# Performance work log

Measured on AMD Instinct MI355X. Metric: run time of the kernel, lower is better.

Reference implementation:

```python
import jax, jax.numpy as jnp
import numpy as np
from jax import lax

B, S, D, F = 2, 4096, 1024, 4096
LN_EPS = 1e-6

def _layer_norm(x, scale, bias):
    mu = jnp.mean(x, axis=-1, keepdims=True)
    var = jnp.mean(jnp.square(x - mu), axis=-1, keepdims=True)
    return (x - mu) * lax.rsqrt(var + LN_EPS) * scale + bias

def _gate_loop(q, k, v, a):
    # max-headed GateLoop: one head per channel, scalar complex state per channel
    # h_t = a_t * h_{t-1} + k_t * v_t ; y_t = q_t * h_t
    kv = (k * v).astype(jnp.complex64)
    def comb(e1, e2):
        a1, x1 = e1
        a2, x2 = e2
        return (a1 * a2, a2 * x1 + x2)
    _, h = lax.associative_scan(comb, (a, kv), axis=1)
    return q.astype(jnp.complex64) * h

def setup_inputs() -> dict:
    key = jax.random.key(0)
    ks = jax.random.split(key, 12)
    sd = 1.0 / np.sqrt(D)
    sf = 1.0 / np.sqrt(F)
    return {
        "x": jax.random.normal(ks[0], (B, S, D), jnp.float32),
        "Wq": jax.random.normal(ks[1], (D, D), jnp.float32) * sd,
        "Wk": jax.random.normal(ks[2], (D, D), jnp.float32) * sd,
        "Wv": jax.random.normal(ks[3], (D, D), jnp.float32) * sd,
        "Wa": jax.random.normal(ks[4], (D, 2 * D), jnp.float32) * sd,
        "Wg": jax.random.normal(ks[5], (D, D), jnp.float32) * sd,
        "Wo": jax.random.normal(ks[6], (D, D), jnp.float32) * sd,
        "ln1_scale": jnp.ones((D,), jnp.float32),
        "ln1_bias": jnp.zeros((D,), jnp.float32),
        "W1": jax.random.normal(ks[7], (D, F), jnp.float32) * sd,
        "b1": jax.random.normal(ks[8], (F,), jnp.float32) * 1e-6,
        "W2": jax.random.normal(ks[9], (F, D), jnp.float32) * sf,
        "b2": jax.random.normal(ks[10], (D,), jnp.float32) * 1e-6,
        "ln2_scale": jnp.ones((D,), jnp.float32),
        "ln2_bias": jnp.zeros((D,), jnp.float32),
    }

def reference(x, Wq, Wk, Wv, Wa, Wg, Wo, ln1_scale, ln1_bias, W1, b1, W2, b2, ln2_scale, ln2_bias):
    q = x @ Wq
    k = x @ Wk
    v = x @ Wv
    a = x @ Wa
    a_real, a_imag = jnp.split(a, 2, axis=-1)
    a_c = a_real + 1j * a_imag
    magnitude = jnp.abs(a_c)
    phase = jnp.angle(a_c)
    a_c = jax.nn.sigmoid(magnitude).astype(jnp.complex64) * jnp.exp(1j * phase)
    g = x.astype(jnp.complex64) @ Wg.astype(jnp.complex64)
    y = _gate_loop(q, k, v, a_c)
    y = y * (g * jax.nn.sigmoid(g))  # silu on complex g
    y = y @ Wo.astype(jnp.complex64)
    y = y.real
    # dropout deterministic (training=False)
    y = _layer_norm(y + x, ln1_scale, ln1_bias)
    h = jax.nn.gelu(y @ W1 + b1)
    out = h @ W2 + b2
    out = _layer_norm(out + y, ln2_scale, ln2_bias)
    return out
```

## Files before the change

### kernel.cpp

```cpp
#include <hip/hip_runtime.h>
#include <cstdint>

typedef unsigned short u16;
typedef unsigned int u32;

#define AS1 __attribute__((address_space(1)))
#define AS3 __attribute__((address_space(3)))

typedef _Float16 f16x8 __attribute__((ext_vector_type(8)));
typedef float f32x4 __attribute__((ext_vector_type(4)));

static constexpr int Bb = 2, Ss = 4096, Dd = 1024, Ff = 4096;
static constexpr int Mtok = Bb * Ss;
static constexpr int NCH = 128;
static constexpr int TCH = Ss / NCH;
static constexpr int PW = 6144;

__device__ __forceinline__ float h2f(u16 u) {
    union { u16 u; _Float16 h; } w; w.u = u; return (float)w.h;
}
__device__ __forceinline__ u16 f2h(float f) {
    union { _Float16 h; u16 u; } w; w.h = (_Float16)f; return w.u;
}

__device__ __forceinline__ void gload_lds16(const u16* g, u16* l) {
    __builtin_amdgcn_global_load_lds((const AS1 u32*)g, (AS3 u32*)l, 16, 0, 0);
}

__global__ __launch_bounds__(256) void cvt_f32_f16(const float* __restrict__ src,
                                                   u16* __restrict__ dst) {
    const long i = ((long)blockIdx.x * 256 + threadIdx.x) * 4;
    float4 f = *(const float4*)(src + i);
    ushort4 o;
    o.x = f2h(f.x); o.y = f2h(f.y); o.z = f2h(f.z); o.w = f2h(f.w);
    *(ushort4*)(dst + i) = o;
}

__global__ __launch_bounds__(1024) void transpose_f32_f16(const float* __restrict__ src,
                                                          u16* __restrict__ dst,
                                                          int K, int N) {
    __shared__ u16 t[32][33];
    const int tx = threadIdx.x, ty = threadIdx.y;
    const int n0 = blockIdx.x * 32, k0 = blockIdx.y * 32;
    t[ty][tx] = f2h(src[(long)(k0 + ty) * N + n0 + tx]);
    __syncthreads();
    dst[(long)(n0 + ty) * K + k0 + tx] = t[tx][ty];
}

template <int EPI>
__global__ __launch_bounds__(512, 2) void gemm8p(const u16* __restrict__ A,
                                                 const u16* __restrict__ BT,
                                                 u16* __restrict__ C,
                                                 const float* __restrict__ bias,
                                                 int M, int N, int K,
                                                 int lda, int ldc) {
    extern __shared__ u16 lds[];
    const int tid = threadIdx.x;

    const int ntn = N >> 8;
    int bid = blockIdx.x;
    {
        const int cpx = gridDim.x >> 3;
        bid = (bid & 7) * cpx + (bid >> 3);
    }
    const int tm = (bid / ntn) << 8;
    const int tn = (bid % ntn) << 8;

    const int srow = tid >> 3;
    const int scol = ((tid & 7) ^ (srow & 7)) << 3;
    const u16* Abase = A + (long)(tm + srow) * lda + scol;
    const u16* Bbase = BT + (long)(tn + srow) * (long)K + scol;
    const long lda64 = (long)lda << 6;
    const long ldb64 = (long)K << 6;

    const int nt = K >> 6;

    auto stA = [&](u16* bufbase, int h, int kt) {
        u16* d = bufbase + h * 8192 + tid * 8;
        const u16* g = Abase + (long)(h * 128) * lda + (kt << 6);
        gload_lds16(g, d);
        gload_lds16(g + lda64, d + 4096);
    };
    auto stB = [&](u16* bufbase, int h, int kt) {
        u16* d = bufbase + 16384 + h * 8192 + tid * 8;
        const u16* g = Bbase + (long)(h * 128) * (long)K + (kt << 6);
        gload_lds16(g, d);
        gload_lds16(g + ldb64, d + 4096);
    };

    const int wid = tid >> 6, lane = tid & 63;
    const int r16 = lane & 15, q = lane >> 4;
    const int wm = (wid >> 2) * 128;
    const int wn = (wid & 3) * 64;
    const int r7 = r16 & 7;
    const int cx0 = (q ^ r7) << 3;
    const int cx1 = ((4 | q) ^ r7) << 3;
    const int aoff = (wm + r16) * 64;
    const int boff = 16384 + (wn + r16) * 64;

    f32x4 acc[8][4];
#pragma unroll
    for (int i = 0; i < 8; i++)
#pragma unroll
        for (int j = 0; j < 4; j++) acc[i][j] = (f32x4){0.f, 0.f, 0.f, 0.f};

    {
        const int t1 = nt > 1 ? 1 : 0;
        stA(lds, 0, 0);
        stA(lds, 1, 0);
        stB(lds, 0, 0);
        stB(lds, 1, 0);
        stB(lds + 32768, 0, t1);
        stB(lds + 32768, 1, t1);
    }

    for (int it = 0; it < nt; ++it) {
        u16* sb = lds + ((it & 1) << 15);
        u16* so = lds + (((it & 1) ^ 1) << 15);
        const int tA = (it + 1 < nt) ? it + 1 : nt - 1;
        const int tB = (it + 2 < nt) ? it + 2 : nt - 1;

        asm volatile("s_waitcnt vmcnt(4)" ::: "memory");
        __builtin_amdgcn_s_barrier();

        f16x8 vb[4][2];
#pragma unroll
        for (int ni = 0; ni < 4; ni++) {
            vb[ni][0] = *(const f16x8*)(sb + boff + ni * 1024 + cx0);
            vb[ni][1] = *(const f16x8*)(sb + boff + ni * 1024 + cx1);
        }

#pragma unroll
        for (int p = 0; p < 4; ++p) {
            f16x8 pa[2][2];
#pragma unroll
            for (int m2 = 0; m2 < 2; m2++) {
                pa[m2][0] = *(const f16x8*)(sb + aoff + (2 * p + m2) * 1024 + cx0);
                pa[m2][1] = *(const f16x8*)(sb + aoff + (2 * p + m2) * 1024 + cx1);
            }
            if (p == 0)      stA(so, 0, tA);
            else if (p == 1) stA(so, 1, tA);
            else if (p == 2) stB(sb, 0, tB);
            else             stB(sb, 1, tB);
            __builtin_amdgcn_s_barrier();
            asm volatile("s_waitcnt lgkmcnt(0)" ::: "memory");
            __builtin_amdgcn_s_setprio(1);
#pragma unroll
            for (int m2 = 0; m2 < 2; m2++)
#pragma unroll
                for (int ni = 0; ni < 4; ni++) {
                    acc[2 * p + m2][ni] = __builtin_amdgcn_mfma_f32_16x16x32_f16(
                        pa[m2][0], vb[ni][0], acc[2 * p + m2][ni], 0, 0, 0);
                    acc[2 * p + m2][ni] = __builtin_amdgcn_mfma_f32_16x16x32_f16(
                        pa[m2][1], vb[ni][1], acc[2 * p + m2][ni], 0, 0, 0);
                }
            __builtin_amdgcn_s_setprio(0);
            __builtin_amdgcn_s_barrier();
        }
    }

    asm volatile("s_waitcnt vmcnt(0)" ::: "memory");

#pragma unroll
    for (int mi = 0; mi < 8; mi++) {
#pragma unroll
        for (int ni = 0; ni < 4; ni++) {
            const int gcol = tn + wn + ni * 16 + r16;
            float bv = 0.f;
            if (EPI) bv = bias[gcol];
#pragma unroll
            for (int j = 0; j < 4; j++) {
                const int grow = tm + wm + mi * 16 + q * 4 + j;
                float v = acc[mi][ni][j];
                if (EPI) v += bv;
                if (EPI == 1) {
                    float t = tanhf(0.7978845608028654f * (v + 0.044715f * v * v * v));
                    v = 0.5f * v * (1.0f + t);
                }
                C[(long)grow * ldc + gcol] = f2h(v);
            }
        }
    }
}

template <int EPI>
__global__ __launch_bounds__(512, 2) void gemm8p_n128(const u16* __restrict__ A,
                                                      const u16* __restrict__ BT,
                                                      u16* __restrict__ C,
                                                      const float* __restrict__ bias,
                                                      int M, int N, int K,
                                                      int lda, int ldc) {
    extern __shared__ u16 lds[];
    const int tid = threadIdx.x;

    const int ntn = N >> 7;
    int bid = blockIdx.x;
    {
        const int cpx = gridDim.x >> 3;
        bid = (bid & 7) * cpx + (bid >> 3);
    }
    const int tm = (bid / ntn) << 8;
    const int tn = (bid % ntn) << 7;

    const int srow = tid >> 3;
    const int scol = ((tid & 7) ^ (srow & 7)) << 3;
    const u16* Abase = A + (long)(tm + srow) * lda + scol;
    const u16* Bbase = BT + (long)(tn + srow) * (long)K + scol;
    const long lda64 = (long)lda << 6;
    const long ldb64 = (long)K << 6;

    const int nt = K >> 6;

    auto stA = [&](u16* bufbase, int h, int kt) {
        u16* d = bufbase + h * 8192 + tid * 8;
        const u16* g = Abase + (long)(h * 128) * lda + (kt << 6);
        gload_lds16(g, d);
        gload_lds16(g + lda64, d + 4096);
    };
    auto stB = [&](u16* bufbase, int kt) {
        u16* d = bufbase + 16384 + tid * 8;
        const u16* g = Bbase + (kt << 6);
        gload_lds16(g, d);
        gload_lds16(g + ldb64, d + 4096);
    };

    const int wid = tid >> 6, lane = tid & 63;
    const int r16 = lane & 15, q = lane >> 4;
    const int wm = (wid >> 1) * 64;
    const int wn = (wid & 1) * 64;
    const int r7 = r16 & 7;
    const int cx0 = (q ^ r7) << 3;
    const int cx1 = ((4 | q) ^ r7) << 3;
    const int aoff = (wm + r16) * 64;
    const int boff = 16384 + (wn + r16) * 64;

    f32x4 acc[4][4];
#pragma unroll
    for (int i = 0; i < 4; i++)
#pragma unroll
        for (int j = 0; j < 4; j++) acc[i][j] = (f32x4){0.f, 0.f, 0.f, 0.f};

    {
        const int t1 = nt > 1 ? 1 : 0;
        stA(lds, 0, 0);
        stA(lds, 1, 0);
        stB(lds, 0);
        stB(lds + 24576, t1);
    }

    for (int it = 0; it < nt; ++it) {
        u16* sb = lds + (it & 1) * 24576;
        u16* so = lds + ((it & 1) ^ 1) * 24576;
        const int tA = (it + 1 < nt) ? it + 1 : nt - 1;
        const int tB = (it + 2 < nt) ? it + 2 : nt - 1;

        asm volatile("s_waitcnt vmcnt(2)" ::: "memory");
        __builtin_amdgcn_s_barrier();

        f16x8 vb[4][2];
#pragma unroll
        for (int ni = 0; ni < 4; ni++) {
            vb[ni][0] = *(const f16x8*)(sb + boff + ni * 1024 + cx0);
            vb[ni][1] = *(const f16x8*)(sb + boff + ni * 1024 + cx1);
        }

#pragma unroll
        for (int p = 0; p < 2; ++p) {
            f16x8 pa[2][2];
#pragma unroll
            for (int m2 = 0; m2 < 2; m2++) {
                pa[m2][0] = *(const f16x8*)(sb + aoff + (2 * p + m2) * 1024 + cx0);
                pa[m2][1] = *(const f16x8*)(sb + aoff + (2 * p + m2) * 1024 + cx1);
            }
            if (p == 0) {
                stA(so, 0, tA);
            } else {
                stA(so, 1, tA);
                stB(sb, tB);
            }
            __builtin_amdgcn_s_barrier();
            asm volatile("s_waitcnt lgkmcnt(0)" ::: "memory");
            __builtin_amdgcn_s_setprio(1);
#pragma unroll
            for (int m2 = 0; m2 < 2; m2++)
#pragma unroll
                for (int ni = 0; ni < 4; ni++) {
                    acc[2 * p + m2][ni] = __builtin_amdgcn_mfma_f32_16x16x32_f16(
                        pa[m2][0], vb[ni][0], acc[2 * p + m2][ni], 0, 0, 0);
                    acc[2 * p + m2][ni] = __builtin_amdgcn_mfma_f32_16x16x32_f16(
                        pa[m2][1], vb[ni][1], acc[2 * p + m2][ni], 0, 0, 0);
                }
            __builtin_amdgcn_s_setprio(0);
            __builtin_amdgcn_s_barrier();
        }
    }

    asm volatile("s_waitcnt vmcnt(0)" ::: "memory");

#pragma unroll
    for (int mi = 0; mi < 4; mi++) {
#pragma unroll
        for (int ni = 0; ni < 4; ni++) {
            const int gcol = tn + wn + ni * 16 + r16;
            float bv = 0.f;
            if (EPI) bv = bias[gcol];
#pragma unroll
            for (int j = 0; j < 4; j++) {
                const int grow = tm + wm + mi * 16 + q * 4 + j;
                float v = acc[mi][ni][j];
                if (EPI) v += bv;
                if (EPI == 1) {
                    float t = tanhf(0.7978845608028654f * (v + 0.044715f * v * v * v));
                    v = 0.5f * v * (1.0f + t);
                }
                C[(long)grow * ldc + gcol] = f2h(v);
            }
        }
    }
}

__device__ __forceinline__ void a_transform(float ar, float ai, float& cr, float& ci) {
    float m = sqrtf(ar * ar + ai * ai);
    float sg = 1.f / (1.f + __expf(-m));
    float sc = sg / fmaxf(m, 1e-30f);
    cr = ar * sc;
    ci = ai * sc;
}

__global__ __launch_bounds__(1024) void scan1(const u16* __restrict__ pcat,
                                              float4* __restrict__ sum4) {
    const int b = blockIdx.y, c = blockIdx.x, d = threadIdx.x;
    float Arp = 1.f, Aip = 0.f, Xr = 0.f, Xi = 0.f;
    const long rowbase = (long)b * Ss + (long)c * TCH;
#pragma unroll 4
    for (int s = 0; s < TCH; ++s) {
        const long ro = (rowbase + s) * PW;
        float ar = h2f(pcat[ro + 3072 + d]);
        float ai = h2f(pcat[ro + 4096 + d]);
        float kk = h2f(pcat[ro + 1024 + d]);
        float vv = h2f(pcat[ro + 2048 + d]);
        float cr, ci;
        a_transform(ar, ai, cr, ci);
        float kv = kk * vv;
        float nXr = cr * Xr - ci * Xi + kv;
        float nXi = cr * Xi + ci * Xr;
        Xr = nXr; Xi = nXi;
        float nAr = cr * Arp - ci * Aip;
        float nAi = cr * Aip + ci * Arp;
        Arp = nAr; Aip = nAi;
    }
    sum4[((long)b * NCH + c) * 1024 + d] = make_float4(Arp, Aip, Xr, Xi);
}

__global__ __launch_bounds__(256) void scan2(const float4* __restrict__ sum4,
                                             float2* __restrict__ carry) {
    const int idx = blockIdx.x * 256 + threadIdx.x;
    const int b = idx >> 10, d = idx & 1023;
    float hr = 0.f, hi = 0.f;
    for (int cb = 0; cb < NCH / 8; ++cb) {
        float4 t[8];
#pragma unroll
        for (int j = 0; j < 8; j++)
            t[j] = sum4[((long)b * NCH + cb * 8 + j) * 1024 + d];
#pragma unroll
        for (int j = 0; j < 8; j++) {
            carry[((long)b * NCH + cb * 8 + j) * 1024 + d] = make_float2(hr, hi);
            float nr = t[j].x * hr - t[j].y * hi + t[j].z;
            float ni = t[j].x * hi + t[j].y * hr + t[j].w;
            hr = nr; hi = ni;
        }
    }
}

__global__ __launch_bounds__(1024) void scan3(u16* pcat,
                                              const float2* __restrict__ carry) {
    const int b = blockIdx.y, c = blockIdx.x, d = threadIdx.x;
    float2 h0 = carry[((long)b * NCH + c) * 1024 + d];
    float hr = h0.x, hi = h0.y;
    const long rowbase = (long)b * Ss + (long)c * TCH;
#pragma unroll 4
    for (int s = 0; s < TCH; ++s) {
        const long ro = (rowbase + s) * PW;
        float ar = h2f(pcat[ro + 3072 + d]);
        float ai = h2f(pcat[ro + 4096 + d]);
        float kk = h2f(pcat[ro + 1024 + d]);
        float vv = h2f(pcat[ro + 2048 + d]);
        float cr, ci;
        a_transform(ar, ai, cr, ci);
        float kv = kk * vv;
        float nhr = cr * hr - ci * hi + kv;
        float nhi = cr * hi + ci * hr;
        hr = nhr; hi = nhi;
        float gg = h2f(pcat[ro + 5120 + d]);
        float si = gg / (1.f + __expf(-gg));
        float yv = h2f(pcat[ro + d]) * hr * si;
        pcat[ro + d] = f2h(yv);
    }
}

template <int RESF32, int OUTF32>
__global__ __launch_bounds__(256) void ln_kernel(const u16* __restrict__ a, int sa,
                                                 const void* __restrict__ bres, int sres,
                                                 const float* __restrict__ scale,
                                                 const float* __restrict__ bias,
                                                 void* __restrict__ out, int sout) {
    const int row = blockIdx.x;
    const int tid = threadIdx.x;
    const long abase = (long)row * sa;
    const long rbase = (long)row * sres;
    const long obase = (long)row * sout;
    float v[4];
#pragma unroll
    for (int j = 0; j < 4; j++) {
        int d = tid * 4 + j;
        float rb = RESF32 ? ((const float*)bres)[rbase + d]
                          : h2f(((const u16*)bres)[rbase + d]);
        v[j] = h2f(a[abase + d]) + rb;
    }
    float s = v[0] + v[1] + v[2] + v[3];
    float s2 = v[0] * v[0] + v[1] * v[1] + v[2] * v[2] + v[3] * v[3];
#pragma unroll
    for (int off = 32; off; off >>= 1) {
        s += __shfl_down(s, off);
        s2 += __shfl_down(s2, off);
    }
    __shared__ float red[8];
    const int w = tid >> 6, lane = tid & 63;
    if (lane == 0) { red[w] = s; red[4 + w] = s2; }
    __syncthreads();
    if (tid == 0) {
        float ts = red[0] + red[1] + red[2] + red[3];
        float ts2 = red[4] + red[5] + red[6] + red[7];
        float mu = ts * (1.f / 1024.f);
        float var = ts2 * (1.f / 1024.f) - mu * mu;
        red[0] = mu;
        red[1] = rsqrtf(var + 1e-6f);
    }
    __syncthreads();
    const float mu = red[0], rs = red[1];
#pragma unroll
    for (int j = 0; j < 4; j++) {
        int d = tid * 4 + j;
        float y = (v[j] - mu) * rs * scale[d] + bias[d];
        if (OUTF32) ((float*)out)[obase + d] = y;
        else        ((u16*)out)[obase + d] = f2h(y);
    }
}

extern "C" void kernel_launch(void* const* d_in, const int* in_sizes, int n_in,
                              void* d_out, int out_size, void* d_ws, size_t ws_size,
                              hipStream_t stream) {
    const float* x    = (const float*)d_in[0];
    const float* Wq   = (const float*)d_in[1];
    const float* Wk   = (const float*)d_in[2];
    const float* Wv   = (const float*)d_in[3];
    const float* Wa   = (const float*)d_in[4];
    const float* Wg   = (const float*)d_in[5];
    const float* Wo   = (const float*)d_in[6];
    const float* ln1s = (const float*)d_in[7];
    const float* ln1b = (const float*)d_in[8];
    const float* W1   = (const float*)d_in[9];
    const float* b1   = (const float*)d_in[10];
    const float* W2   = (const float*)d_in[11];
    const float* b2   = (const float*)d_in[12];
    const float* ln2s = (const float*)d_in[13];
    const float* ln2b = (const float*)d_in[14];

    u16* ws    = (u16*)d_ws;
    u16* xb    = ws;
    u16* WTcat = xb + (8u << 20);
    u16* WTo   = WTcat + (6u << 20);
    u16* WT1   = WTo + (1u << 20);
    u16* WT2   = WT1 + (4u << 20);
    u16* pcat  = WT2 + (4u << 20);

    float4* sum4  = (float4*)WTcat;
    float2* carry = (float2*)(WTcat + (2u << 20));

    static bool attr_done = false;
    if (!attr_done) {
        hipFuncSetAttribute(reinterpret_cast<const void*>(&gemm8p<0>),
                            hipFuncAttributeMaxDynamicSharedMemorySize, 131072);
        hipFuncSetAttribute(reinterpret_cast<const void*>(&gemm8p<1>),
                            hipFuncAttributeMaxDynamicSharedMemorySize, 131072);
        hipFuncSetAttribute(reinterpret_cast<const void*>(&gemm8p_n128<0>),
                            hipFuncAttributeMaxDynamicSharedMemorySize, 98304);
        hipFuncSetAttribute(reinterpret_cast<const void*>(&gemm8p_n128<2>),
                            hipFuncAttributeMaxDynamicSharedMemorySize, 98304);
        attr_done = true;
    }


    cvt_f32_f16<<<dim3(8192), dim3(256), 0, stream>>>(x, xb);

    const dim3 tb(32, 32);
    transpose_f32_f16<<<dim3(32, 32), tb, 0, stream>>>(Wq, WTcat, 1024, 1024);
    transpose_f32_f16<<<dim3(32, 32), tb, 0, stream>>>(Wk, WTcat + (1u << 20), 1024, 1024);
    transpose_f32_f16<<<dim3(32, 32), tb, 0, stream>>>(Wv, WTcat + (2u << 20), 1024, 1024);
    transpose_f32_f16<<<dim3(64, 32), tb, 0, stream>>>(Wa, WTcat + (3u << 20), 1024, 2048);
    transpose_f32_f16<<<dim3(32, 32), tb, 0, stream>>>(Wg, WTcat + (5u << 20), 1024, 1024);
    transpose_f32_f16<<<dim3(32, 32), tb, 0, stream>>>(Wo, WTo, 1024, 1024);
    transpose_f32_f16<<<dim3(128, 32), tb, 0, stream>>>(W1, WT1, 1024, 4096);
    transpose_f32_f16<<<dim3(32, 128), tb, 0, stream>>>(W2, WT2, 4096, 1024);

    gemm8p<0><<<dim3(768), dim3(512), 131072, stream>>>(xb, WTcat, pcat, nullptr,
                                                        Mtok, PW, 1024, 1024, PW);
    scan1<<<dim3(NCH, Bb), 1024, 0, stream>>>(pcat, sum4);
    scan2<<<dim3(8), 256, 0, stream>>>(sum4, carry);
    scan3<<<dim3(NCH, Bb), 1024, 0, stream>>>(pcat, carry);
    gemm8p_n128<0><<<dim3(256), dim3(512), 98304, stream>>>(pcat, WTo, pcat + 1024,
                                                            nullptr,
                                                            Mtok, 1024, 1024, PW, PW);
    ln_kernel<1, 0><<<dim3(Mtok), dim3(256), 0, stream>>>(pcat + 1024, PW, x, 1024,
                                                          ln1s, ln1b, pcat, PW);
    gemm8p<1><<<dim3(512), dim3(512), 131072, stream>>>(pcat, WT1, pcat + 2048, b1,
                                                        Mtok, Ff, 1024, PW, PW);
    gemm8p_n128<2><<<dim3(256), dim3(512), 98304, stream>>>(pcat + 2048, WT2,
                                                            pcat + 1024, b2,
                                                            Mtok, 1024, Ff, PW, PW);
    ln_kernel<0, 1><<<dim3(Mtok), dim3(256), 0, stream>>>(pcat + 1024, PW, pcat, PW,
                                                          ln2s, ln2b, d_out, 1024);
}
```

Before: 565.6 us.

## Make 256-wide GEMM persistent with cross-tile prefetch and fuse prep kernels

Result: faster. 528.1 us (-6.6%).

```diff
diff --git a/kernel.cpp b/kernel.cpp
--- a/kernel.cpp
+++ b/kernel.cpp
@@ -27,24 +27,49 @@
     __builtin_amdgcn_global_load_lds((const AS1 u32*)g, (AS3 u32*)l, 16, 0, 0);
 }
 
-__global__ __launch_bounds__(256) void cvt_f32_f16(const float* __restrict__ src,
-                                                   u16* __restrict__ dst) {
-    const long i = ((long)blockIdx.x * 256 + threadIdx.x) * 4;
-    float4 f = *(const float4*)(src + i);
-    ushort4 o;
-    o.x = f2h(f.x); o.y = f2h(f.y); o.z = f2h(f.z); o.w = f2h(f.w);
-    *(ushort4*)(dst + i) = o;
-}
-
-__global__ __launch_bounds__(1024) void transpose_f32_f16(const float* __restrict__ src,
-                                                          u16* __restrict__ dst,
-                                                          int K, int N) {
+__global__ __launch_bounds__(256) void prep_fused(
+    const float* __restrict__ x, u16* __restrict__ xb,
+    const float* __restrict__ Wq, const float* __restrict__ Wk,
+    const float* __restrict__ Wv, const float* __restrict__ Wa,
+    const float* __restrict__ Wg, const float* __restrict__ Wo,
+    const float* __restrict__ W1, const float* __restrict__ W2,
+    u16* __restrict__ WTcat, u16* __restrict__ WTo,
+    u16* __restrict__ WT1, u16* __restrict__ WT2) {
     __shared__ u16 t[32][33];
-    const int tx = threadIdx.x, ty = threadIdx.y;
-    const int n0 = blockIdx.x * 32, k0 = blockIdx.y * 32;
-    t[ty][tx] = f2h(src[(long)(k0 + ty) * N + n0 + tx]);
+    const int tid = threadIdx.x;
+    const int idx = blockIdx.x;
+    if (idx < 8192) {
+        const long i = ((long)idx * 256 + tid) * 4;
+        float4 f = *(const float4*)(x + i);
+        ushort4 o;
+        o.x = f2h(f.x); o.y = f2h(f.y); o.z = f2h(f.z); o.w = f2h(f.w);
+        *(ushort4*)(xb + i) = o;
+        return;
+    }
+    const float* src; u16* dst; int K, N, ti;
+    if (idx < 9216)       { src = Wq; dst = WTcat;             K = 1024; N = 1024; ti = idx - 8192; }
+    else if (idx < 10240) { src = Wk; dst = WTcat + (1u << 20); K = 1024; N = 1024; ti = idx - 9216; }
+    else if (idx < 11264) { src = Wv; dst = WTcat + (2u << 20); K = 1024; N = 1024; ti = idx - 10240; }
+    else if (idx < 13312) { src = Wa; dst = WTcat + (3u << 20); K = 1024; N = 2048; ti = idx - 11264; }
+    else if (idx < 14336) { src = Wg; dst = WTcat + (5u << 20); K = 1024; N = 1024; ti = idx - 13312; }
+    else if (idx < 15360) { src = Wo; dst = WTo;               K = 1024; N = 1024; ti = idx - 14336; }
+    else if (idx < 19456) { src = W1; dst = WT1;               K = 1024; N = 4096; ti = idx - 15360; }
+    else                  { src = W2; dst = WT2;               K = 4096; N = 1024; ti = idx - 19456; }
+    const int tiles_x = N >> 5;
+    const int bx = ti % tiles_x, by = ti / tiles_x;
+    const int n0 = bx << 5, k0 = by << 5;
+    const int tx = tid & 31, ty = tid >> 5;
+#pragma unroll
+    for (int r = 0; r < 4; r++) {
+        const int row = ty + r * 8;
+        t[row][tx] = f2h(src[(long)(k0 + row) * N + n0 + tx]);
+    }
     __syncthreads();
-    dst[(long)(n0 + ty) * K + k0 + tx] = t[tx][ty];
+#pragma unroll
+    for (int r = 0; r < 4; r++) {
+        const int row = ty + r * 8;
+        dst[(long)(n0 + row) * K + k0 + tx] = t[tx][row];
+    }
 }
 
 template <int EPI>
@@ -58,32 +83,36 @@
     const int tid = threadIdx.x;
 
     const int ntn = N >> 8;
-    int bid = blockIdx.x;
-    {
-        const int cpx = gridDim.x >> 3;
-        bid = (bid & 7) * cpx + (bid >> 3);
-    }
-    const int tm = (bid / ntn) << 8;
-    const int tn = (bid % ntn) << 8;
+    const int total = (M >> 8) * ntn;
+    const int tpb = total / (int)gridDim.x;
+    const int cpx = total >> 3;
 
     const int srow = tid >> 3;
     const int scol = ((tid & 7) ^ (srow & 7)) << 3;
-    const u16* Abase = A + (long)(tm + srow) * lda + scol;
-    const u16* Bbase = BT + (long)(tn + srow) * (long)K + scol;
     const long lda64 = (long)lda << 6;
     const long ldb64 = (long)K << 6;
 
     const int nt = K >> 6;
 
-    auto stA = [&](u16* bufbase, int h, int kt) {
+    auto bases_for = [&](int t, int& tm, int& tn, const u16*& Ab, const u16*& Bb) {
+        if (t > tpb - 1) t = tpb - 1;
+        const int ti = (int)blockIdx.x + t * (int)gridDim.x;
+        const int b = (ti & 7) * cpx + (ti >> 3);
+        tm = (b / ntn) << 8;
+        tn = (b % ntn) << 8;
+        Ab = A + (long)(tm + srow) * lda + scol;
+        Bb = BT + (long)(tn + srow) * (long)K + scol;
+    };
+
+    auto stA = [&](u16* bufbase, int h, const u16* Ab, int kt) {
         u16* d = bufbase + h * 8192 + tid * 8;
-        const u16* g = Abase + (long)(h * 128) * lda + (kt << 6);
+        const u16* g = Ab + (long)(h * 128) * lda + (kt << 6);
         gload_lds16(g, d);
         gload_lds16(g + lda64, d + 4096);
     };
-    auto stB = [&](u16* bufbase, int h, int kt) {
+    auto stB = [&](u16* bufbase, int h, const u16* Bb, int kt) {
         u16* d = bufbase + 16384 + h * 8192 + tid * 8;
-        const u16* g = Bbase + (long)(h * 128) * (long)K + (kt << 6);
+        const u16* g = Bb + (long)(h * 128) * (long)K + (kt << 6);
         gload_lds16(g, d);
         gload_lds16(g + ldb64, d + 4096);
     };
@@ -104,83 +133,97 @@
 #pragma unroll
         for (int j = 0; j < 4; j++) acc[i][j] = (f32x4){0.f, 0.f, 0.f, 0.f};
 
-    {
-        const int t1 = nt > 1 ? 1 : 0;
-        stA(lds, 0, 0);
-        stA(lds, 1, 0);
-        stB(lds, 0, 0);
-        stB(lds, 1, 0);
-        stB(lds + 32768, 0, t1);
-        stB(lds + 32768, 1, t1);
-    }
-
-    for (int it = 0; it < nt; ++it) {
-        u16* sb = lds + ((it & 1) << 15);
-        u16* so = lds + (((it & 1) ^ 1) << 15);
-        const int tA = (it + 1 < nt) ? it + 1 : nt - 1;
-        const int tB = (it + 2 < nt) ? it + 2 : nt - 1;
-
-        asm volatile("s_waitcnt vmcnt(4)" ::: "memory");
-        __builtin_amdgcn_s_barrier();
-
-        f16x8 vb[4][2];
-#pragma unroll
-        for (int ni = 0; ni < 4; ni++) {
-            vb[ni][0] = *(const f16x8*)(sb + boff + ni * 1024 + cx0);
-            vb[ni][1] = *(const f16x8*)(sb + boff + ni * 1024 + cx1);
-        }
-
-#pragma unroll
-        for (int p = 0; p < 4; ++p) {
-            f16x8 pa[2][2];
-#pragma unroll
-            for (int m2 = 0; m2 < 2; m2++) {
-                pa[m2][0] = *(const f16x8*)(sb + aoff + (2 * p + m2) * 1024 + cx0);
-                pa[m2][1] = *(const f16x8*)(sb + aoff + (2 * p + m2) * 1024 + cx1);
+    int tmc, tnc, tmn, tnn;
+    const u16 *Ac, *Bc, *An, *Bn;
+    bases_for(0, tmc, tnc, Ac, Bc);
+    bases_for(1, tmn, tnn, An, Bn);
+
+    stA(lds, 0, Ac, 0);
+    stA(lds, 1, Ac, 0);
+    stB(lds, 0, Bc, 0);
+    stB(lds, 1, Bc, 0);
+    stB(lds + 32768, 0, Bc, 1);
+    stB(lds + 32768, 1, Bc, 1);
+
+    for (int t = 0; t < tpb; ++t) {
+        for (int it = 0; it < nt; ++it) {
+            u16* sb = lds + ((it & 1) << 15);
+            u16* so = lds + (((it & 1) ^ 1) << 15);
+
+            asm volatile("s_waitcnt vmcnt(4)" ::: "memory");
+            __builtin_amdgcn_s_barrier();
+
+            f16x8 vb[4][2];
+#pragma unroll
+            for (int ni = 0; ni < 4; ni++) {
+                vb[ni][0] = *(const f16x8*)(sb + boff + ni * 1024 + cx0);
+                vb[ni][1] = *(const f16x8*)(sb + boff + ni * 1024 + cx1);
             }
-            if (p == 0)      stA(so, 0, tA);
-            else if (p == 1) stA(so, 1, tA);
-            else if (p == 2) stB(sb, 0, tB);
-            else             stB(sb, 1, tB);
-            __builtin_amdgcn_s_barrier();
-            asm volatile("s_waitcnt lgkmcnt(0)" ::: "memory");
-            __builtin_amdgcn_s_setprio(1);
-#pragma unroll
-            for (int m2 = 0; m2 < 2; m2++)
-#pragma unroll
-                for (int ni = 0; ni < 4; ni++) {
-                    acc[2 * p + m2][ni] = __builtin_amdgcn_mfma_f32_16x16x32_f16(
-                        pa[m2][0], vb[ni][0], acc[2 * p + m2][ni], 0, 0, 0);
-                    acc[2 * p + m2][ni] = __builtin_amdgcn_mfma_f32_16x16x32_f16(
-                        pa[m2][1], vb[ni][1], acc[2 * p + m2][ni], 0, 0, 0);
+
+#pragma unroll
+            for (int p = 0; p < 4; ++p) {
+                f16x8 pa[2][2];
+#pragma unroll
+                for (int m2 = 0; m2 < 2; m2++) {
+                    pa[m2][0] = *(const f16x8*)(sb + aoff + (2 * p + m2) * 1024 + cx0);
+                    pa[m2][1] = *(const f16x8*)(sb + aoff + (2 * p + m2) * 1024 + cx1);
                 }
-            __builtin_amdgcn_s_setprio(0);
-            __builtin_amdgcn_s_barrier();
-        }
-    }
-
-    asm volatile("s_waitcnt vmcnt(0)" ::: "memory");
-
-#pragma unroll
-    for (int mi = 0; mi < 8; mi++) {
-#pragma unroll
-        for (int ni = 0; ni < 4; ni++) {
-            const int gcol = tn + wn + ni * 16 + r16;
-            float bv = 0.f;
-            if (EPI) bv = bias[gcol];
-#pragma unroll
-            for (int j = 0; j < 4; j++) {
-                const int grow = tm + wm + mi * 16 + q * 4 + j;
-                float v = acc[mi][ni][j];
-                if (EPI) v += bv;
-                if (EPI == 1) {
-                    float t = tanhf(0.7978845608028654f * (v + 0.044715f * v * v * v));
-                    v = 0.5f * v * (1.0f + t);
+                if (p == 0) {
+                    if (it + 1 < nt) stA(so, 0, Ac, it + 1);
+                    else             stA(so, 0, An, 0);
+                } else if (p == 1) {
+                    if (it + 1 < nt) stA(so, 1, Ac, it + 1);
+                    else             stA(so, 1, An, 0);
+                } else if (p == 2) {
+                    if (it + 2 < nt) stB(sb, 0, Bc, it + 2);
+                    else             stB(sb, 0, Bn, it + 2 - nt);
+                } else {
+                    if (it + 2 < nt) stB(sb, 1, Bc, it + 2);
+                    else             stB(sb, 1, Bn, it + 2 - nt);
                 }
-                C[(long)grow * ldc + gcol] = f2h(v);
+                __builtin_amdgcn_s_barrier();
+                asm volatile("s_waitcnt lgkmcnt(0)" ::: "memory");
+                __builtin_amdgcn_s_setprio(1);
+#pragma unroll
+                for (int m2 = 0; m2 < 2; m2++)
+#pragma unroll
+                    for (int ni = 0; ni < 4; ni++) {
+                        acc[2 * p + m2][ni] = __builtin_amdgcn_mfma_f32_16x16x32_f16(
+                            pa[m2][0], vb[ni][0], acc[2 * p + m2][ni], 0, 0, 0);
+                        acc[2 * p + m2][ni] = __builtin_amdgcn_mfma_f32_16x16x32_f16(
+                            pa[m2][1], vb[ni][1], acc[2 * p + m2][ni], 0, 0, 0);
+                    }
+                __builtin_amdgcn_s_setprio(0);
+                __builtin_amdgcn_s_barrier();
             }
         }
-    }
+
+#pragma unroll
+        for (int mi = 0; mi < 8; mi++) {
+#pragma unroll
+            for (int ni = 0; ni < 4; ni++) {
+                const int gcol = tnc + wn + ni * 16 + r16;
+                float bv = 0.f;
+                if (EPI) bv = bias[gcol];
+#pragma unroll
+                for (int j = 0; j < 4; j++) {
+                    const int grow = tmc + wm + mi * 16 + q * 4 + j;
+                    float v = acc[mi][ni][j];
+                    if (EPI) v += bv;
+                    if (EPI == 1) {
+                        float tt = tanhf(0.7978845608028654f * (v + 0.044715f * v * v * v));
+                        v = 0.5f * v * (1.0f + tt);
+                    }
+                    C[(long)grow * ldc + gcol] = f2h(v);
+                    acc[mi][ni][j] = 0.f;
+                }
+            }
+        }
+        tmc = tmn; tnc = tnn; Ac = An; Bc = Bn;
+        bases_for(t + 2, tmn, tnn, An, Bn);
+    }
+
+    asm volatile("s_waitcnt vmcnt(0)" ::: "memory");
 }
 
 template <int EPI>
@@ -491,19 +534,10 @@
     }
 
 
-    cvt_f32_f16<<<dim3(8192), dim3(256), 0, stream>>>(x, xb);
-
-    const dim3 tb(32, 32);
-    transpose_f32_f16<<<dim3(32, 32), tb, 0, stream>>>(Wq, WTcat, 1024, 1024);
-    transpose_f32_f16<<<dim3(32, 32), tb, 0, stream>>>(Wk, WTcat + (1u << 20), 1024, 1024);
-    transpose_f32_f16<<<dim3(32, 32), tb, 0, stream>>>(Wv, WTcat + (2u << 20), 1024, 1024);
-    transpose_f32_f16<<<dim3(64, 32), tb, 0, stream>>>(Wa, WTcat + (3u << 20), 1024, 2048);
-    transpose_f32_f16<<<dim3(32, 32), tb, 0, stream>>>(Wg, WTcat + (5u << 20), 1024, 1024);
-    transpose_f32_f16<<<dim3(32, 32), tb, 0, stream>>>(Wo, WTo, 1024, 1024);
-    transpose_f32_f16<<<dim3(128, 32), tb, 0, stream>>>(W1, WT1, 1024, 4096);
-    transpose_f32_f16<<<dim3(32, 128), tb, 0, stream>>>(W2, WT2, 4096, 1024);
-
-    gemm8p<0><<<dim3(768), dim3(512), 131072, stream>>>(xb, WTcat, pcat, nullptr,
+    prep_fused<<<dim3(23552), dim3(256), 0, stream>>>(x, xb, Wq, Wk, Wv, Wa, Wg, Wo,
+                                                      W1, W2, WTcat, WTo, WT1, WT2);
+
+    gemm8p<0><<<dim3(256), dim3(512), 131072, stream>>>(xb, WTcat, pcat, nullptr,
                                                         Mtok, PW, 1024, 1024, PW);
     scan1<<<dim3(NCH, Bb), 1024, 0, stream>>>(pcat, sum4);
     scan2<<<dim3(8), 256, 0, stream>>>(sum4, carry);
@@ -513,7 +547,7 @@
                                                             Mtok, 1024, 1024, PW, PW);
     ln_kernel<1, 0><<<dim3(Mtok), dim3(256), 0, stream>>>(pcat + 1024, PW, x, 1024,
                                                           ln1s, ln1b, pcat, PW);
-    gemm8p<1><<<dim3(512), dim3(512), 131072, stream>>>(pcat, WT1, pcat + 2048, b1,
+    gemm8p<1><<<dim3(256), dim3(512), 131072, stream>>>(pcat, WT1, pcat + 2048, b1,
                                                         Mtok, Ff, 1024, PW, PW);
     gemm8p_n128<2><<<dim3(256), dim3(512), 98304, stream>>>(pcat + 2048, WT2,
                                                             pcat + 1024, b2,
```
